# Kernel tuning notes

Hardware: AMD Instinct MI355X
Metric: run time of the kernel (lower is better)

Reference implementation:

```python
import jax, jax.numpy as jnp
import numpy as np

B, T, D, H, K = 4, 1024, 768, 12, 64
DMIX, DDEC = 32, 64

def setup_inputs() -> dict:
    key = jax.random.key(0)
    ks = jax.random.split(key, 24)
    def n(k, shape, s=1.0):
        return jax.random.normal(k, shape, dtype=jnp.float32) * s
    return {
        "x": n(ks[0], (B, T, D)),
        "time_maa_x": n(ks[1], (1, 1, D), 0.1) + 0.5,
        "time_maa_w": n(ks[2], (1, 1, D), 0.1) + 0.5,
        "time_maa_k": n(ks[3], (1, 1, D), 0.1) + 0.5,
        "time_maa_v": n(ks[4], (1, 1, D), 0.1) + 0.5,
        "time_maa_r": n(ks[5], (1, 1, D), 0.1) + 0.5,
        "time_maa_g": n(ks[6], (1, 1, D), 0.1) + 0.5,
        "maa_w1": n(ks[7], (D, 5 * DMIX), 0.01),
        "maa_w2": n(ks[8], (5, DMIX, D), 0.01),
        "time_decay": jnp.linspace(-6.0, -1.0, D).reshape(1, 1, D).astype(jnp.float32),
        "decay_w1": n(ks[9], (D, DDEC), 0.01),
        "decay_w2": n(ks[10], (DDEC, D), 0.01),
        "lucid_temp": jnp.ones((1, H, 1, 1), jnp.float32),
        "Wr": n(ks[11], (D, D), 0.02),
        "Wk": n(ks[12], (D, D), 0.02),
        "Wv": n(ks[13], (D, D), 0.02),
        "Wg": n(ks[14], (D, D), 0.02),
        "Wo": n(ks[15], (D, D), 0.02),
        "ln_w": jnp.ones((D,), jnp.float32),
        "ln_b": jnp.zeros((D,), jnp.float32),
    }

def reference(x, time_maa_x, time_maa_w, time_maa_k, time_maa_v, time_maa_r, time_maa_g,
              maa_w1, maa_w2, time_decay, decay_w1, decay_w2, lucid_temp,
              Wr, Wk, Wv, Wg, Wo, ln_w, ln_b):
    Bb, Tt, Dd = x.shape
    Hh = lucid_temp.shape[1]
    Kk = Dd // Hh
    # bidirectional token shift: average of left/right neighbors
    left = jnp.pad(x[:, :-1], ((0, 0), (1, 0), (0, 0)))
    right = jnp.pad(x[:, 1:], ((0, 0), (0, 1), (0, 0)))
    dxprev = 0.5 * (left + right) - x
    # data-dependent mixing coefficients (5-way low-rank)
    xxx = x + dxprev * time_maa_x
    m = jnp.tanh(xxx @ maa_w1).reshape(Bb, Tt, 5, DMIX)
    mm = jnp.einsum('btcd,cde->cbte', m, maa_w2)  # (5,B,T,D)
    mw, mk, mv, mr, mg = mm[0], mm[1], mm[2], mm[3], mm[4]
    xw = x + dxprev * (time_maa_w + mw)
    xk = x + dxprev * (time_maa_k + mk)
    xv = x + dxprev * (time_maa_v + mv)
    xr = x + dxprev * (time_maa_r + mr)
    xg = x + dxprev * (time_maa_g + mg)
    r = xr @ Wr
    k = xk @ Wk
    v = xv @ Wv
    g = jax.nn.silu(xg @ Wg)
    w = time_decay + jnp.tanh(xw @ decay_w1) @ decay_w2
    def heads(t):
        return t.reshape(Bb, Tt, Hh, Kk).transpose(0, 2, 1, 3)  # (B,H,T,K)
    r_h, k_h, v_h = heads(r), heads(k), heads(v)
    w_h = -jnp.exp(heads(w))
    # LION bidirectional decay attention
    cs = jnp.cumsum(w_h, axis=2)
    cs_b = cs - w_h
    cs_f_s = jnp.clip(cs - cs[:, :, Tt // 2:Tt // 2 + 1, :], -60.0, 60.0)
    cs_b_s = jnp.clip(cs_b - cs_b[:, :, Tt // 2:Tt // 2 + 1, :], -60.0, 60.0)
    A_fwd = jnp.tril(jnp.einsum('bhtk,bhsk->bhts', r_h * jnp.exp(cs_f_s), k_h * jnp.exp(-cs_f_s)))
    A_bwd = jnp.triu(jnp.einsum('bhtk,bhsk->bhts', r_h * jnp.exp(-cs_b_s), k_h * jnp.exp(cs_b_s)), 1)
    A = A_fwd + A_bwd
    # LUCID preconditioner: solve (I + exp(temp * K_norm K_norm^T)) Pv = v
    kn = k_h / jnp.maximum(jnp.linalg.norm(k_h, axis=-1, keepdims=True), 1e-12)
    gram = jnp.einsum('bhtk,bhsk->bhts', kn, kn)
    temp = jax.nn.softplus(lucid_temp)
    P = jnp.eye(Tt, dtype=jnp.float32) + jnp.exp(jnp.clip(temp * gram, -20.0, 20.0))
    Pv = jnp.linalg.solve(P, v_h)
    y = jnp.einsum('bhts,bhsk->bhtk', A, Pv)
    # GroupNorm over heads (groups = H, eps = 1e-5 * head_size_divisor^2)
    y = y.transpose(0, 2, 1, 3)  # (B,T,H,K)
    eps = 1e-5 * 64.0
    mu = y.mean(axis=-1, keepdims=True)
    var = y.var(axis=-1, keepdims=True)
    yn = (y - mu) / jnp.sqrt(var + eps)
    yn = yn.reshape(Bb, Tt, Dd) * ln_w + ln_b
    return (yn * g) @ Wo
```

## Files before the change

kernel.cpp:

```cpp
#include <hip/hip_runtime.h>
#include <math.h>

#define CB 4
#define CT 1024
#define CD 768
#define CH 12
#define CK 64
#define CBH (CB*CH)
#define NB 64

#define PTILE(i,j) ((size_t)(((i)*((i)+1))/2 + (j))*4096)
#define PBF ((size_t)136*4096)

typedef __attribute__((ext_vector_type(8))) short sh8;
typedef __attribute__((ext_vector_type(8))) unsigned short ush8;
typedef __attribute__((ext_vector_type(4))) unsigned short ush4;
typedef __attribute__((ext_vector_type(4))) float fl4;

__device__ __forceinline__ unsigned short f2bf(float f){
    unsigned u = __builtin_bit_cast(unsigned, f);
    unsigned r = (u + 0x7fff + ((u >> 16) & 1)) >> 16;
    return (unsigned short)r;
}
__device__ __forceinline__ float bf2f(unsigned short u){
    return __builtin_bit_cast(float, (unsigned)u << 16);
}
#define MFMA3(acc, ah, al, bh_, bl_) { \
    acc = __builtin_amdgcn_mfma_f32_16x16x32_bf16(al, bh_, acc, 0, 0, 0); \
    acc = __builtin_amdgcn_mfma_f32_16x16x32_bf16(ah, bl_, acc, 0, 0, 0); \
    acc = __builtin_amdgcn_mfma_f32_16x16x32_bf16(ah, bh_, acc, 0, 0, 0); }

#define LOAD_TILE(dst, src, stride) { \
    _Pragma("unroll") \
    for (int i_ = 0; i_ < 4; i_++){ \
        int rr_ = (tid>>4) + i_*16, cc_ = (tid&15)*4; \
        float4 v_ = *(const float4*)((src) + (size_t)rr_*(stride) + cc_); \
        dst[rr_][cc_+0]=v_.x; dst[rr_][cc_+1]=v_.y; dst[rr_][cc_+2]=v_.z; dst[rr_][cc_+3]=v_.w; \
    } }

__global__ void k_shift(const float* __restrict__ x, const float* __restrict__ tmx,
                        float* __restrict__ dxprev, float* __restrict__ xxx){
    int idx = blockIdx.x*256 + threadIdx.x;
    if (idx >= CB*CT*CD) return;
    int d = idx % CD;
    int bt = idx / CD;
    int t = bt % CT;
    float xc = x[idx];
    float xl = (t > 0)      ? x[idx - CD] : 0.f;
    float xr = (t < CT-1)   ? x[idx + CD] : 0.f;
    float dx = 0.5f*(xl + xr) - xc;
    dxprev[idx] = dx;
    xxx[idx] = xc + dx * tmx[d];
}

template<int MODE>
__global__ void k_gemm(const float* __restrict__ A, const float* __restrict__ Bm,
                       const float* __restrict__ bias, float* __restrict__ C,
                       int M, int N, int Kd){
    __shared__ float As[16][128];
    __shared__ float Bs[16][64];
    int tid = threadIdx.x;
    int m0 = blockIdx.y * 128, n0 = blockIdx.x * 64;
    int tn = (tid & 15) * 4;
    int tm = (tid >> 4) * 8;
    float acc[8][4] = {};
    for (int k0 = 0; k0 < Kd; k0 += 16){
        #pragma unroll
        for (int i = 0; i < 8; i++){
            int e = tid + i*256;
            int r = e >> 4, c = e & 15;
            As[c][r] = A[(size_t)(m0+r)*Kd + k0 + c];
        }
        #pragma unroll
        for (int i = 0; i < 4; i++){
            int e = tid + i*256;
            int r = e >> 6, c = e & 63;
            float bv = 0.f;
            if (n0 + c < N) bv = Bm[(size_t)(k0+r)*N + n0 + c];
            Bs[r][c] = bv;
        }
        __syncthreads();
        #pragma unroll
        for (int kk = 0; kk < 16; kk++){
            float a0[8], b0[4];
// ... 228 lines not shown
                       float* __restrict__ P, int bh0){
    int ti = blockIdx.y, tj = blockIdx.x;
    if (ti < tj) return;
    int t0 = ti*64, s0 = tj*64;
    __shared__ float tA[64][65];
    __shared__ float tB[64][65];
    int lbh = blockIdx.z; int gbh = bh0 + lbh; int h = gbh % CH;
    int tid = threadIdx.x;
    LOAD_TILE(tA, kn + ((size_t)gbh*CT + t0)*64, 64);
    LOAD_TILE(tB, kn + ((size_t)gbh*CT + s0)*64, 64);
    __syncthreads();
    float tv = lucid_temp[h];
    tv = (tv > 20.f) ? tv : log1pf(expf(tv));
    int ty = (tid >> 4)*4, tx = (tid & 15)*4;
    float acc[4][4] = {};
    #pragma unroll
    for (int kk = 0; kk < 64; kk++){
        float a0[4], b0[4];
        #pragma unroll
        for (int i = 0; i < 4; i++){ a0[i] = tA[ty+i][kk]; b0[i] = tB[tx+i][kk]; }
        #pragma unroll
        for (int i = 0; i < 4; i++)
            #pragma unroll
            for (int j = 0; j < 4; j++) acc[i][j] += a0[i]*b0[j];
    }
    float* Pt = P + (size_t)lbh*PBF + PTILE(ti,tj);
    #pragma unroll
    for (int i = 0; i < 4; i++){
        int tt = t0+ty+i;
        float4 v;
        float g0 = fminf(fmaxf(tv*acc[i][0], -20.f), 20.f);
        float g1 = fminf(fmaxf(tv*acc[i][1], -20.f), 20.f);
        float g2 = fminf(fmaxf(tv*acc[i][2], -20.f), 20.f);
        float g3 = fminf(fmaxf(tv*acc[i][3], -20.f), 20.f);
        v.x = expf(g0) + ((tt == s0+tx+0) ? 1.f : 0.f);
        v.y = expf(g1) + ((tt == s0+tx+1) ? 1.f : 0.f);
        v.z = expf(g2) + ((tt == s0+tx+2) ? 1.f : 0.f);
        v.w = expf(g3) + ((tt == s0+tx+3) ? 1.f : 0.f);
        *(float4*)(Pt + (size_t)(ty+i)*64 + tx) = v;
    }
}

__device__ __forceinline__ void potrf_inv(float (&s)[64][65], float (&inv)[64][65], int tid){
    for (int j = 0; j < 63; j++){
        __syncthreads();
        float invd = 1.f / fmaxf(s[j][j], 1e-20f);
        int n = 63 - j;
        for (int e = tid; e < n*n; e += 256){
            int ii = j+1 + e / n, cc = j+1 + e % n;
            s[ii][cc] -= s[ii][j]*s[cc][j]*invd;
        }
    }
    __syncthreads();
    for (int e = tid; e < 64*64; e += 256){
        int i2 = e >> 6, j2 = e & 63;
        if (i2 > j2) s[i2][j2] *= rsqrtf(fmaxf(s[j2][j2], 1e-20f));
    }
    __syncthreads();
    if (tid < 64) s[tid][tid] = sqrtf(fmaxf(s[tid][tid], 1e-20f));
    __syncthreads();
    if (tid < 64){
        int c = tid;
        for (int j = 0; j < c; j++) inv[j][c] = 0.f;
        for (int j = c; j < 64; j++){
            float sum = (j == c) ? 1.f : 0.f;
            for (int kk = c; kk < j; kk++) sum -= s[j][kk]*inv[kk][c];
            inv[j][c] = sum / s[j][j];
        }
    }
    __syncthreads();
}

__device__ __forceinline__ void potrf_writeout(float (&s)[64][65], float (&inv)[64][65], int tid,
                                               float* __restrict__ Pd, float* __restrict__ invp){
    for (int e = tid; e < 4096; e += 256){
        int r2 = e >> 6, c2 = e & 63;
        if (c2 <= r2) Pd[(size_t)r2*64 + c2] = s[r2][c2];
    }
    #pragma unroll
    for (int i_ = 0; i_ < 4; i_++){
        int rr_ = (tid>>4) + i_*16, cc_ = (tid&15)*4;
        float4 v_ = make_float4(inv[rr_][cc_], inv[rr_][cc_+1], inv[rr_][cc_+2], inv[rr_][cc_+3]);
        *(float4*)(invp + rr_*64 + cc_) = v_;
    }
}

__global__ void k_potrf0(float* __restrict__ P, float* __restrict__ invL){
    __shared__ float s[64][65], inv[64][65];
    int bh = blockIdx.x; int tid = threadIdx.x;
    float* Pt = P + (size_t)bh*PBF;
    LOAD_TILE(s, Pt, 64);
    __syncthreads();
    potrf_inv(s, inv, tid);
    potrf_writeout(s, inv, tid, Pt, invL + (size_t)bh*16*4096);
}

__global__ void k_trsm(float* __restrict__ P, const float* __restrict__ invL, int jb){
    __shared__ float a[64][65];
    __shared__ float iv[64][65];
    int bh = blockIdx.y;
    int rt = jb + 1 + blockIdx.x;
    int tid = threadIdx.x;
    float* Pt = P + (size_t)bh*PBF + PTILE(rt,jb);
    const float* invp = invL + ((size_t)bh*16 + jb)*4096;
    LOAD_TILE(a, Pt, 64);
    LOAD_TILE(iv, invp, 64);
    __syncthreads();
    int ty = (tid >> 4)*4, tx = (tid & 15)*4;
    float acc[4][4] = {};
    #pragma unroll
    for (int kk = 0; kk < 64; kk++){
        float a0[4], b0[4];
        #pragma unroll
        for (int i = 0; i < 4; i++){ a0[i] = a[ty+i][kk]; b0[i] = iv[tx+i][kk]; }
        #pragma unroll
        for (int i = 0; i < 4; i++)
            #pragma unroll
            for (int j = 0; j < 4; j++) acc[i][j] += a0[i]*b0[j];
    }
    #pragma unroll
    for (int i = 0; i < 4; i++)
        *(float4*)(Pt + (size_t)(ty+i)*64 + tx) =
            make_float4(acc[i][0], acc[i][1], acc[i][2], acc[i][3]);
}

__global__ void k_syrkf(float* __restrict__ P, float* __restrict__ invL,
                        float* __restrict__ X, float* __restrict__ Yb, int bh0, int jb){
    __shared__ float sA[64][65], sB[64][65], sC[64][65];
    int tj = blockIdx.x, ti = blockIdx.y, lbh = blockIdx.z;
    int tid = threadIdx.x;
    int ty = (tid >> 4)*4, tx = (tid & 15)*4;
    float* Pb = P + (size_t)lbh*PBF;
    if (tj == gridDim.x - 1){
        int ib = jb + 1 + ti;
        const float* invp = invL + ((size_t)lbh*16 + jb)*4096;
        const float* Xj = X + ((size_t)(bh0+lbh)*CT + jb*64)*64;
        LOAD_TILE(sA, invp, 64);
        LOAD_TILE(sB, Xj, 64);
        __syncthreads();
        float c4[4][4] = {};
        #pragma unroll
        for (int kk = 0; kk < 64; kk++){
            float a0[4], b0[4];
            #pragma unroll
            for (int i = 0; i < 4; i++){ a0[i] = sA[ty+i][kk]; b0[i] = sB[kk][tx+i]; }
            #pragma unroll
            for (int i = 0; i < 4; i++)
                #pragma unroll
                for (int j = 0; j < 4; j++) c4[i][j] += a0[i]*b0[j];
        }
        if (ti == 0){
            float* yd = Yb + ((size_t)(bh0+lbh)*CT + jb*64)*64;
            #pragma unroll
            for (int i = 0; i < 4; i++)
                *(float4*)(yd + (size_t)(ty+i)*64 + tx) =
                    make_float4(c4[i][0], c4[i][1], c4[i][2], c4[i][3]);
        }
        #pragma unroll
        for (int i = 0; i < 4; i++)
            #pragma unroll
            for (int j = 0; j < 4; j++) sC[ty+i][tx+j] = c4[i][j];
        __syncthreads();
        LOAD_TILE(sA, Pb + PTILE(ib,jb), 64);
        __syncthreads();
        float u4[4][4] = {};
        #pragma unroll
        for (int kk = 0; kk < 64; kk++){
            float a0[4], b0[4];
            #pragma unroll
            for (int i = 0; i < 4; i++){ a0[i] = sA[ty+i][kk]; b0[i] = sC[kk][tx+i]; }
            #pragma unroll
            for (int i = 0; i < 4; i++)
                #pragma unroll
                for (int j = 0; j < 4; j++) u4[i][j] += a0[i]*b0[j];
        }
        float* dst = X + ((size_t)(bh0+lbh)*CT + ib*64)*64;
        #pragma unroll
        for (int i = 0; i < 4; i++){
            float4* p4 = (float4*)(dst + (size_t)(ty+i)*64 + tx);
            float4 v = *p4;
            v.x -= u4[i][0]; v.y -= u4[i][1]; v.z -= u4[i][2]; v.w -= u4[i][3];
            *p4 = v;
        }
        return;
    }
    if (tj > ti) return;
    int ibr = jb + 1 + ti, ibc = jb + 1 + tj;
    LOAD_TILE(sA, Pb + PTILE(ibr,jb), 64);
    LOAD_TILE(sB, Pb + PTILE(ibc,jb), 64);
    __syncthreads();
    float acc[4][4] = {};
    #pragma unroll
    for (int kk = 0; kk < 64; kk++){
        float a0[4], b0[4];
        #pragma unroll
        for (int i = 0; i < 4; i++){ a0[i] = sA[ty+i][kk]; b0[i] = sB[tx+i][kk]; }
        #pragma unroll
        for (int i = 0; i < 4; i++)
            #pragma unroll
            for (int j = 0; j < 4; j++) acc[i][j] += a0[i]*b0[j];
    }
    if (!(ti == 0 && tj == 0)){
        float* Pt = Pb + PTILE(ibr,ibc);
        #pragma unroll
        for (int i = 0; i < 4; i++){
            float4* p4 = (float4*)(Pt + (size_t)(ty+i)*64 + tx);
            float4 v = *p4;
            v.x -= acc[i][0]; v.y -= acc[i][1]; v.z -= acc[i][2]; v.w -= acc[i][3];
            *p4 = v;
        }
    } else {
        float* Pt = Pb + PTILE(ibr,ibr);
        __syncthreads();
        #pragma unroll
        for (int i = 0; i < 4; i++){
            float4 v = *(const float4*)(Pt + (size_t)(ty+i)*64 + tx);
            sA[ty+i][tx+0] = v.x - acc[i][0];
            sA[ty+i][tx+1] = v.y - acc[i][1];
            sA[ty+i][tx+2] = v.z - acc[i][2];
            sA[ty+i][tx+3] = v.w - acc[i][3];
        }
        __syncthreads();
        potrf_inv(sA, sB, tid);
        potrf_writeout(sA, sB, tid, Pt, invL + ((size_t)lbh*16 + jb+1)*4096);
    }
}

template<int TRANS>
__global__ void k_solve(const float* __restrict__ P, const float* __restrict__ invL,
                        float* __restrict__ Xc, float* __restrict__ Yb, int bh0, int jb){
    __shared__ float A[64][65], B[64][65], C[64][65];
    int bh = blockIdx.y, tid = threadIdx.x;
    int ib = TRANS ? blockIdx.x : (jb + blockIdx.x);
    const float* invp = invL + ((size_t)bh*16 + jb)*4096;
    const float* src = (TRANS ? Yb : Xc) + ((size_t)(bh0+bh)*CT + jb*64)*64;
    LOAD_TILE(A, invp, 64);
    LOAD_TILE(B, src, 64);
    __syncthreads();
    int ty = (tid >> 4)*4, tx = (tid & 15)*4;
    float c4[4][4] = {};
    #pragma unroll
    for (int kk = 0; kk < 64; kk++){
        float a0[4], b0[4];
        #pragma unroll
        for (int i = 0; i < 4; i++){
            a0[i] = TRANS ? A[kk][ty+i] : A[ty+i][kk];
            b0[i] = B[kk][tx+i];
        }
        #pragma unroll
        for (int i = 0; i < 4; i++)
            #pragma unroll
            for (int j = 0; j < 4; j++) c4[i][j] += a0[i]*b0[j];
    }
    if (ib == jb){
        float* dst = (TRANS ? Xc : Yb) + ((size_t)(bh0+bh)*CT + jb*64)*64;
        #pragma unroll
        for (int i = 0; i < 4; i++)
            *(float4*)(dst + (size_t)(ty+i)*64 + tx) =
                make_float4(c4[i][0], c4[i][1], c4[i][2], c4[i][3]);
        return;
    }
    #pragma unroll
    for (int i = 0; i < 4; i++)
        #pragma unroll
        for (int j = 0; j < 4; j++) C[ty+i][tx+j] = c4[i][j];
    __syncthreads();
    const float* Lp = P + (size_t)bh*PBF + (TRANS ? PTILE(jb,ib) : PTILE(ib,jb));
    LOAD_TILE(A, Lp, 64);
    __syncthreads();
    float u4[4][4] = {};
    #pragma unroll
    for (int kk = 0; kk < 64; kk++){
        float a0[4], b0[4];
        #pragma unroll
        for (int i = 0; i < 4; i++){
            a0[i] = TRANS ? A[kk][ty+i] : A[ty+i][kk];
            b0[i] = C[kk][tx+i];
        }
        #pragma unroll
        for (int i = 0; i < 4; i++)
            #pragma unroll
            for (int j = 0; j < 4; j++) u4[i][j] += a0[i]*b0[j];
    }
    float* dst = (TRANS ? Yb : Xc) + ((size_t)(bh0+bh)*CT + ib*64)*64;
    #pragma unroll
    for (int i = 0; i < 4; i++){
        float4* p4 = (float4*)(dst + (size_t)(ty+i)*64 + tx);
        float4 v = *p4;
        v.x -= u4[i][0]; v.y -= u4[i][1]; v.z -= u4[i][2]; v.w -= u4[i][3];
        *p4 = v;
    }
}

__global__ void k_outer(const float* __restrict__ kf, const float* __restrict__ kb,
                        const float* __restrict__ X,
                        float* __restrict__ Sf, float* __restrict__ Sb){
    __shared__ float kfs[64][65], kbs[64][65], pvs[64][65];
    int c = blockIdx.x, bh = blockIdx.y, tid = threadIdx.x;
    size_t hb = (size_t)bh*CT*64 + (size_t)c*64*64;
    LOAD_TILE(kfs, kf + hb, 64);
    LOAD_TILE(kbs, kb + hb, 64);
    LOAD_TILE(pvs, X + hb, 64);
    __syncthreads();
    int ty = (tid >> 4)*4, tx = (tid & 15)*4;
    float af[4][4] = {}, ab[4][4] = {};
    #pragma unroll
    for (int kk = 0; kk < 64; kk++){
        float f0[4], g0[4], b0[4];
        #pragma unroll
        for (int i = 0; i < 4; i++){
            f0[i] = kfs[kk][ty+i];
            g0[i] = kbs[kk][ty+i];
            b0[i] = pvs[kk][tx+i];
        }
        #pragma unroll
        for (int i = 0; i < 4; i++)
            #pragma unroll
            for (int j = 0; j < 4; j++){
                af[i][j] += f0[i]*b0[j];
                ab[i][j] += g0[i]*b0[j];
            }
    }
    size_t sb = ((size_t)bh*16 + c)*4096;
    #pragma unroll
    for (int i = 0; i < 4; i++){
        *(float4*)(Sf + sb + (size_t)(ty+i)*64 + tx) = make_float4(af[i][0], af[i][1], af[i][2], af[i][3]);
        *(float4*)(Sb + sb + (size_t)(ty+i)*64 + tx) = make_float4(ab[i][0], ab[i][1], ab[i][2], ab[i][3]);
    }
}

__global__ void k_cumsum(float* __restrict__ Sf, float* __restrict__ Sb){
    int bh = blockIdx.x, tid = threadIdx.x;
    size_t base = (size_t)bh*16*4096;
    #pragma unroll
    for (int i = 0; i < 16; i++){
        int e = tid + i*256;
        float run = 0.f;
        for (int c = 0; c < 16; c++){
            float* p = Sf + base + (size_t)c*4096 + e;
            float t = *p; *p = run; run += t;
        }
        run = 0.f;
        for (int c = 15; c >= 0; c--){
            float* p = Sb + base + (size_t)c*4096 + e;
            float t = *p; *p = run; run += t;
        }
    }
}

__global__ void k_apv2(const float* __restrict__ rf, const float* __restrict__ kf,
                       const float* __restrict__ rb, const float* __restrict__ kb,
                       const float* __restrict__ X,
                       const float* __restrict__ Sf, const float* __restrict__ Sb,
                       float* __restrict__ y){
    __shared__ float rs[64][65], ks[64][65], at[64][65];
    int c = blockIdx.x, bh = blockIdx.y, tid = threadIdx.x;
    size_t hb = (size_t)bh*CT*64 + (size_t)c*64*64;
    size_t sb = ((size_t)bh*16 + c)*4096;
    int ty = (tid >> 4)*4, tx = (tid & 15)*4;
    LOAD_TILE(rs, rf + hb, 64);
    LOAD_TILE(ks, kf + hb, 64);
    __syncthreads();
    float a4[4][4] = {};
    #pragma unroll
    for (int kk = 0; kk < 64; kk++){
        float a0[4], b0[4];
        #pragma unroll
        for (int i = 0; i < 4; i++){ a0[i] = rs[ty+i][kk]; b0[i] = ks[tx+i][kk]; }
        #pragma unroll
        for (int i = 0; i < 4; i++)
            #pragma unroll
            for (int j = 0; j < 4; j++) a4[i][j] += a0[i]*b0[j];
    }
    __syncthreads();
// ... 44 lines not shown
            #pragma unroll
            for (int j = 0; j < 4; j++) yacc[i][j] += a0[i]*b0[j];
    }
    __syncthreads();
    LOAD_TILE(rs, Sb + sb, 64);
    LOAD_TILE(ks, rb + hb, 64);
    __syncthreads();
    #pragma unroll 8
    for (int kk = 0; kk < 64; kk++){
        float a0[4], b0[4];
        #pragma unroll
        for (int i = 0; i < 4; i++){ a0[i] = ks[ty+i][kk]; b0[i] = rs[kk][tx+i]; }
        #pragma unroll
        for (int i = 0; i < 4; i++)
            #pragma unroll
            for (int j = 0; j < 4; j++) yacc[i][j] += a0[i]*b0[j];
    }
    #pragma unroll
    for (int i = 0; i < 4; i++)
        *(float4*)(y + hb + (size_t)(ty+i)*64 + tx) =
            make_float4(yacc[i][0], yacc[i][1], yacc[i][2], yacc[i][3]);
}

__global__ void k_gn(const float* __restrict__ y, const float* __restrict__ g,
                     const float* __restrict__ lnw, const float* __restrict__ lnb,
                     float* __restrict__ z){
    int gw = (blockIdx.x*256 + threadIdx.x) >> 6;
    int lane = threadIdx.x & 63;
    if (gw >= CB*CT*CH) return;
    int h = gw % CH; int bt = gw / CH;
    int b = bt / CT, t = bt % CT;
    int bh = b*CH + h;
    float yv = y[((size_t)bh*CT + t)*64 + lane];
    float s1 = yv, s2 = yv*yv;
    #pragma unroll
    for (int off = 32; off; off >>= 1){ s1 += __shfl_xor(s1, off); s2 += __shfl_xor(s2, off); }
    float mu = s1 * (1.f/64.f);
    float var = s2 * (1.f/64.f) - mu*mu;
    float inv = rsqrtf(var + 6.4e-4f);
    int d = h*64 + lane;
    float yn = (yv - mu)*inv*lnw[d] + lnb[d];
    z[(size_t)bt*CD + d] = yn * g[(size_t)bt*CD + d];
}

extern "C" void kernel_launch(void* const* d_in, const int* in_sizes, int n_in,
                              void* d_out, int out_size, void* d_ws, size_t ws_size,
                              hipStream_t stream){
    const float* x          = (const float*)d_in[0];
    const float* tmx        = (const float*)d_in[1];
    const float* tmw        = (const float*)d_in[2];
    const float* tmk        = (const float*)d_in[3];
    const float* tmv        = (const float*)d_in[4];
    const float* tmr        = (const float*)d_in[5];
    const float* tmg        = (const float*)d_in[6];
    const float* maa_w1     = (const float*)d_in[7];
    const float* maa_w2     = (const float*)d_in[8];
    const float* time_decay = (const float*)d_in[9];
    const float* decay_w1   = (const float*)d_in[10];
    const float* decay_w2   = (const float*)d_in[11];
    const float* lucid_temp = (const float*)d_in[12];
    const float* Wr         = (const float*)d_in[13];
    const float* Wk         = (const float*)d_in[14];
    const float* Wv         = (const float*)d_in[15];
    const float* Wg         = (const float*)d_in[16];
    const float* Wo         = (const float*)d_in[17];
    const float* lnw        = (const float*)d_in[18];
    const float* lnb        = (const float*)d_in[19];
    float* out = (float*)d_out;
    float* ws  = (float*)d_ws;

    const size_t S = (size_t)CB*CT*CD;
    float* b0 = ws;
    float* b1 = ws + 1*S;
    float* b2 = ws + 2*S;
    float* b3 = ws + 3*S;
    float* b4 = ws + 4*S;
    float* b5 = ws + 5*S;
    float* b6 = ws + 6*S;
    float* b7 = ws + 7*S;
    float* b8 = ws + 8*S;
    float* b9 = ws + 9*S;
    float* mbuf = ws + 10*S;
    const size_t MB_F = 4096*160;
    size_t base_f = 10*S + MB_F;

    const size_t per_bh = PBF + 16*4096;
    size_t avail = ws_size / sizeof(float);
    int G = 1;
    if (avail > base_f + per_bh){
        size_t g = (avail - base_f) / per_bh;
        G = (g >= CBH) ? CBH : (int)g;
        if (G < 1) G = 1;
    }
    float* P    = ws + base_f;
    float* invL = P + (size_t)G*PBF;

    unsigned short* BtHi = (unsigned short*)P;
    unsigned short* BtLo = BtHi + (size_t)CD*CD;

    float* dxprev = b0; float* xxx = b1;
    float* xw = b1; float* xk = b2; float* xv = b3; float* xr = b4; float* xg = b5;
    float* rbuf = b6; float* kbuf = b7; float* vbuf = b8; float* gbuf = b9; float* wbuf = b0;
    float* kn = b4; float* X = b5;
    float* rf = b1; float* kf = b2; float* rb = b3; float* kb = b8;
    float* Yb = b0;
    float* Sf = b4; float* Sb = b0;
    float* ybuf = b6; float* zbuf = b7;

    dim3 mg(CD/64, (CB*CT)/64);
    dim3 tg(CD/64, CD/64);

    k_shift<<<dim3((CB*CT*CD + 255)/256), 256, 0, stream>>>(x, tmx, dxprev, xxx);
    k_gemm<1><<<dim3(3, 32), 256, 0, stream>>>(xxx, maa_w1, nullptr, mbuf, 4096, 160, 768);
    k_mix5<<<dim3(3, 4096), 256, 0, stream>>>(x, dxprev, mbuf, tmw, tmk, tmv, tmr, tmg,
                                              maa_w2, xw, xk, xv, xr, xg);
    k_splitT<<<tg, 256, 0, stream>>>(Wr, BtHi, BtLo, CD, CD);
    k_mgemm<0><<<mg, 256, 0, stream>>>(xr, BtHi, BtLo, nullptr, rbuf, 4096, CD, CD);
    k_splitT<<<tg, 256, 0, stream>>>(Wk, BtHi, BtLo, CD, CD);
    k_mgemm<0><<<mg, 256, 0, stream>>>(xk, BtHi, BtLo, nullptr, kbuf, 4096, CD, CD);
    k_splitT<<<tg, 256, 0, stream>>>(Wv, BtHi, BtLo, CD, CD);
    k_mgemm<0><<<mg, 256, 0, stream>>>(xv, BtHi, BtLo, nullptr, vbuf, 4096, CD, CD);
    k_splitT<<<tg, 256, 0, stream>>>(Wg, BtHi, BtLo, CD, CD);
    k_mgemm<2><<<mg, 256, 0, stream>>>(xg, BtHi, BtLo, nullptr, gbuf, 4096, CD, CD);
    k_splitT<<<dim3(1, 12), 256, 0, stream>>>(decay_w1, BtHi, BtLo, CD, 64);
    k_mgemm<1><<<dim3(1, 64), 256, 0, stream>>>(xw, BtHi, BtLo, nullptr, mbuf, 4096, 64, CD);
    k_splitT<<<dim3(12, 1), 256, 0, stream>>>(decay_w2, BtHi, BtLo, 64, CD);
    k_mgemm<3><<<dim3(12, 64), 256, 0, stream>>>(mbuf, BtHi, BtLo, time_decay, wbuf, 4096, CD, 64);

    k_knvx<<<dim3((CB*CH*CT*64)/256), 256, 0, stream>>>(kbuf, vbuf, kn, X);
    k_scan2<<<dim3(CBH), 256, 0, stream>>>(rbuf, kbuf, wbuf, rf, kf, rb, kb);

    for (int bh0 = 0; bh0 < CBH; bh0 += G){
        int Gc = (CBH - bh0 < G) ? (CBH - bh0) : G;
        k_gram<<<dim3(16, 16, Gc), 256, 0, stream>>>(kn, lucid_temp, P, bh0);
        k_potrf0<<<dim3(Gc), 256, 0, stream>>>(P, invL);
        for (int jb = 0; jb < 15; jb++){
            int nt = 15 - jb;
            k_trsm<<<dim3(nt, Gc), 256, 0, stream>>>(P, invL, jb);
            k_syrkf<<<dim3(nt+1, nt, Gc), 256, 0, stream>>>(P, invL, X, Yb, bh0, jb);
        }
        k_solve<0><<<dim3(1, Gc), 256, 0, stream>>>(P, invL, X, Yb, bh0, 15);
        for (int jb = 15; jb >= 0; jb--)
            k_solve<1><<<dim3(jb+1, Gc), 256, 0, stream>>>(P, invL, X, Yb, bh0, jb);
    }

    k_outer<<<dim3(16, CBH), 256, 0, stream>>>(kf, kb, X, Sf, Sb);
    k_cumsum<<<dim3(CBH), 256, 0, stream>>>(Sf, Sb);
    k_apv2<<<dim3(16, CBH), 256, 0, stream>>>(rf, kf, rb, kb, X, Sf, Sb, ybuf);
    k_gn<<<dim3((CB*CT*CH*64)/256), 256, 0, stream>>>(ybuf, gbuf, lnw, lnb, zbuf);
    k_splitT<<<tg, 256, 0, stream>>>(Wo, BtHi, BtLo, CD, CD);
    k_mgemm<0><<<mg, 256, 0, stream>>>(zbuf, BtHi, BtLo, nullptr, out, 4096, CD, CD);
}
```

Measured before the change: 3.330 ms.

## Fuse blocked Cholesky and triangular solves into one cooperative persistent kernel

Replaces the sequence of small per-step launches (potrf, trsm, syrk and forward/backward solve per block column) with one cooperative kernel. It loops over phases and uses grid-wide syncs between them, removing many tiny kernel launches and their launch gaps. In exchange, each phase spins on grid barriers, occupancy is limited by three 64x65 shared tiles per block, and the cooperative launch falls back to the old path if it fails.

Result: no change. 3.329 ms (-0.0%).

```diff
diff --git a/kernel.cpp b/kernel.cpp
--- a/kernel.cpp
+++ b/kernel.cpp
@@ -1,5 +1,8 @@
 #include <hip/hip_runtime.h>
+#include <hip/hip_cooperative_groups.h>
 #include <math.h>
+
+namespace cg = cooperative_groups;
 
 #define CB 4
 #define CT 1024
@@ -394,6 +397,240 @@
         int rr_ = (tid>>4) + i_*16, cc_ = (tid&15)*4;
         float4 v_ = make_float4(inv[rr_][cc_], inv[rr_][cc_+1], inv[rr_][cc_+2], inv[rr_][cc_+3]);
         *(float4*)(invp + rr_*64 + cc_) = v_;
+    }
+}
+
+__global__ __launch_bounds__(256) void k_chol(float* __restrict__ P, float* __restrict__ invL,
+                                              float* __restrict__ X, float* __restrict__ Yb,
+                                              int bh0, int Gc){
+    cg::grid_group gg = cg::this_grid();
+    __shared__ float sA[64][65], sB[64][65], sC[64][65];
+    int tid = threadIdx.x;
+    int ty = (tid >> 4)*4, tx = (tid & 15)*4;
+    int NBK = gridDim.x, blk = blockIdx.x;
+
+    for (int t = blk; t < Gc; t += NBK){
+        float* Pt = P + (size_t)t*PBF;
+        LOAD_TILE(sA, Pt, 64);
+        __syncthreads();
+        potrf_inv(sA, sB, tid);
+        potrf_writeout(sA, sB, tid, Pt, invL + (size_t)t*16*4096);
+        __syncthreads();
+    }
+    gg.sync();
+
+    for (int jb = 0; jb < 15; jb++){
+        int nt = 15 - jb;
+        for (int t = blk; t < Gc*nt; t += NBK){
+            int bh = t / nt, ti = t % nt;
+            int rt = jb + 1 + ti;
+            float* Pt = P + (size_t)bh*PBF + PTILE(rt,jb);
+            const float* invp = invL + ((size_t)bh*16 + jb)*4096;
+            LOAD_TILE(sA, Pt, 64);
+            LOAD_TILE(sB, invp, 64);
+            __syncthreads();
+            float acc[4][4] = {};
+            #pragma unroll
+            for (int kk = 0; kk < 64; kk++){
+                float a0[4], b0[4];
+                #pragma unroll
+                for (int i = 0; i < 4; i++){ a0[i] = sA[ty+i][kk]; b0[i] = sB[tx+i][kk]; }
+                #pragma unroll
+                for (int i = 0; i < 4; i++)
+                    #pragma unroll
+                    for (int j = 0; j < 4; j++) acc[i][j] += a0[i]*b0[j];
+            }
+            __syncthreads();
+            #pragma unroll
+            for (int i = 0; i < 4; i++)
+                *(float4*)(Pt + (size_t)(ty+i)*64 + tx) =
+                    make_float4(acc[i][0], acc[i][1], acc[i][2], acc[i][3]);
+        }
+        gg.sync();
+        int Wd = nt + 1;
+        for (int t = blk; t < Gc*nt*Wd; t += NBK){
+            int bh = t / (nt*Wd); int r = t % (nt*Wd);
+            int ti = r / Wd, tj = r % Wd;
+            float* Pb = P + (size_t)bh*PBF;
+            if (tj == nt){
+                int ib = jb + 1 + ti;
+                const float* invp = invL + ((size_t)bh*16 + jb)*4096;
+                const float* Xj = X + ((size_t)(bh0+bh)*CT + jb*64)*64;
+                LOAD_TILE(sA, invp, 64);
+                LOAD_TILE(sB, Xj, 64);
+                __syncthreads();
+                float c4[4][4] = {};
+                #pragma unroll
+                for (int kk = 0; kk < 64; kk++){
+                    float a0[4], b0[4];
+                    #pragma unroll
+                    for (int i = 0; i < 4; i++){ a0[i] = sA[ty+i][kk]; b0[i] = sB[kk][tx+i]; }
+                    #pragma unroll
+                    for (int i = 0; i < 4; i++)
+                        #pragma unroll
+                        for (int j = 0; j < 4; j++) c4[i][j] += a0[i]*b0[j];
+                }
+                if (ti == 0){
+                    float* yd = Yb + ((size_t)(bh0+bh)*CT + jb*64)*64;
+                    #pragma unroll
+                    for (int i = 0; i < 4; i++)
+                        *(float4*)(yd + (size_t)(ty+i)*64 + tx) =
+                            make_float4(c4[i][0], c4[i][1], c4[i][2], c4[i][3]);
+                }
+                #pragma unroll
+                for (int i = 0; i < 4; i++)
+                    #pragma unroll
+                    for (int j = 0; j < 4; j++) sC[ty+i][tx+j] = c4[i][j];
+                __syncthreads();
+                LOAD_TILE(sA, Pb + PTILE(ib,jb), 64);
+                __syncthreads();
+                float u4[4][4] = {};
+                #pragma unroll
+                for (int kk = 0; kk < 64; kk++){
+                    float a0[4], b0[4];
+                    #pragma unroll
+                    for (int i = 0; i < 4; i++){ a0[i] = sA[ty+i][kk]; b0[i] = sC[kk][tx+i]; }
+                    #pragma unroll
+                    for (int i = 0; i < 4; i++)
+                        #pragma unroll
+                        for (int j = 0; j < 4; j++) u4[i][j] += a0[i]*b0[j];
+                }
+                float* dst = X + ((size_t)(bh0+bh)*CT + ib*64)*64;
+                #pragma unroll
+                for (int i = 0; i < 4; i++){
+                    float4* p4 = (float4*)(dst + (size_t)(ty+i)*64 + tx);
+                    float4 v = *p4;
+                    v.x -= u4[i][0]; v.y -= u4[i][1]; v.z -= u4[i][2]; v.w -= u4[i][3];
+                    *p4 = v;
+                }
+                __syncthreads();
+            } else if (tj <= ti){
+                int ibr = jb + 1 + ti, ibc = jb + 1 + tj;
+                LOAD_TILE(sA, Pb + PTILE(ibr,jb), 64);
+                LOAD_TILE(sB, Pb + PTILE(ibc,jb), 64);
+                __syncthreads();
+                float acc[4][4] = {};
+                #pragma unroll
+                for (int kk = 0; kk < 64; kk++){
+                    float a0[4], b0[4];
+                    #pragma unroll
+                    for (int i = 0; i < 4; i++){ a0[i] = sA[ty+i][kk]; b0[i] = sB[tx+i][kk]; }
+                    #pragma unroll
+                    for (int i = 0; i < 4; i++)
+                        #pragma unroll
+                        for (int j = 0; j < 4; j++) acc[i][j] += a0[i]*b0[j];
+                }
+                __syncthreads();
+                if (!(ti == 0 && tj == 0)){
+                    float* Pt = Pb + PTILE(ibr,ibc);
+                    #pragma unroll
+                    for (int i = 0; i < 4; i++){
+                        float4* p4 = (float4*)(Pt + (size_t)(ty+i)*64 + tx);
+                        float4 v = *p4;
+                        v.x -= acc[i][0]; v.y -= acc[i][1]; v.z -= acc[i][2]; v.w -= acc[i][3];
+                        *p4 = v;
+                    }
+                } else {
+                    float* Pt = Pb + PTILE(ibr,ibr);
+                    #pragma unroll
+                    for (int i = 0; i < 4; i++){
+                        float4 v = *(const float4*)(Pt + (size_t)(ty+i)*64 + tx);
+                        sA[ty+i][tx+0] = v.x - acc[i][0];
+                        sA[ty+i][tx+1] = v.y - acc[i][1];
+                        sA[ty+i][tx+2] = v.z - acc[i][2];
+                        sA[ty+i][tx+3] = v.w - acc[i][3];
+                    }
+                    __syncthreads();
+                    potrf_inv(sA, sB, tid);
+                    potrf_writeout(sA, sB, tid, Pt, invL + ((size_t)bh*16 + jb+1)*4096);
+                    __syncthreads();
+                }
+            }
+        }
+        gg.sync();
+    }
+    for (int t = blk; t < Gc; t += NBK){
+        const float* invp = invL + ((size_t)t*16 + 15)*4096;
+        const float* Xj = X + ((size_t)(bh0+t)*CT + 15*64)*64;
+        LOAD_TILE(sA, invp, 64);
+        LOAD_TILE(sB, Xj, 64);
+        __syncthreads();
+        float c4[4][4] = {};
+        #pragma unroll
+        for (int kk = 0; kk < 64; kk++){
+            float a0[4], b0[4];
+            #pragma unroll
+            for (int i = 0; i < 4; i++){ a0[i] = sA[ty+i][kk]; b0[i] = sB[kk][tx+i]; }
+            #pragma unroll
+            for (int i = 0; i < 4; i++)
+                #pragma unroll
+                for (int j = 0; j < 4; j++) c4[i][j] += a0[i]*b0[j];
+        }
+        __syncthreads();
+        float* yd = Yb + ((size_t)(bh0+t)*CT + 15*64)*64;
+        #pragma unroll
+        for (int i = 0; i < 4; i++)
+            *(float4*)(yd + (size_t)(ty+i)*64 + tx) =
+                make_float4(c4[i][0], c4[i][1], c4[i][2], c4[i][3]);
+    }
+    gg.sync();
+    for (int jb = 15; jb >= 0; jb--){
+        for (int t = blk; t < Gc*(jb+1); t += NBK){
+            int bh = t / (jb+1), ib = t % (jb+1);
+            const float* invp = invL + ((size_t)bh*16 + jb)*4096;
+            const float* src = Yb + ((size_t)(bh0+bh)*CT + jb*64)*64;
+            LOAD_TILE(sA, invp, 64);
+            LOAD_TILE(sB, src, 64);
+            __syncthreads();
+            float c4[4][4] = {};
+            #pragma unroll
+            for (int kk = 0; kk < 64; kk++){
+                float a0[4], b0[4];
+                #pragma unroll
+                for (int i = 0; i < 4; i++){ a0[i] = sA[kk][ty+i]; b0[i] = sB[kk][tx+i]; }
+                #pragma unroll
+                for (int i = 0; i < 4; i++)
+                    #pragma unroll
+                    for (int j = 0; j < 4; j++) c4[i][j] += a0[i]*b0[j];
+            }
+            if (ib == jb){
+                float* dst = X + ((size_t)(bh0+bh)*CT + jb*64)*64;
+                #pragma unroll
+                for (int i = 0; i < 4; i++)
+                    *(float4*)(dst + (size_t)(ty+i)*64 + tx) =
+                        make_float4(c4[i][0], c4[i][1], c4[i][2], c4[i][3]);
+                __syncthreads();
+            } else {
+                #pragma unroll
+                for (int i = 0; i < 4; i++)
+                    #pragma unroll
+                    for (int j = 0; j < 4; j++) sC[ty+i][tx+j] = c4[i][j];
+                __syncthreads();
+                LOAD_TILE(sA, P + (size_t)bh*PBF + PTILE(jb,ib), 64);
+                __syncthreads();
+                float u4[4][4] = {};
+                #pragma unroll
+                for (int kk = 0; kk < 64; kk++){
+                    float a0[4], b0[4];
+                    #pragma unroll
+                    for (int i = 0; i < 4; i++){ a0[i] = sA[kk][ty+i]; b0[i] = sC[kk][tx+i]; }
+                    #pragma unroll
+                    for (int i = 0; i < 4; i++)
+                        #pragma unroll
+                        for (int j = 0; j < 4; j++) u4[i][j] += a0[i]*b0[j];
+                }
+                float* dst = Yb + ((size_t)(bh0+bh)*CT + ib*64)*64;
+                #pragma unroll
+                for (int i = 0; i < 4; i++){
+                    float4* p4 = (float4*)(dst + (size_t)(ty+i)*64 + tx);
+                    float4 v = *p4;
+                    v.x -= u4[i][0]; v.y -= u4[i][1]; v.z -= u4[i][2]; v.w -= u4[i][3];
+                    *p4 = v;
+                }
+                __syncthreads();
+            }
+        }
+        gg.sync();
     }
 }
 
@@ -860,18 +1097,39 @@
     k_knvx<<<dim3((CB*CH*CT*64)/256), 256, 0, stream>>>(kbuf, vbuf, kn, X);
     k_scan2<<<dim3(CBH), 256, 0, stream>>>(rbuf, kbuf, wbuf, rf, kf, rb, kb);
 
+    int devId = 0;
+    hipGetDevice(&devId);
+    hipDeviceProp_t prop;
+    hipGetDeviceProperties(&prop, devId);
+    int maxB = 0;
+    hipError_t occErr = hipOccupancyMaxActiveBlocksPerMultiprocessor(&maxB, k_chol, 256, 0);
+    int nblk = (occErr == hipSuccess && maxB > 0) ? maxB * prop.multiProcessorCount : 0;
+    if (nblk > 2048) nblk = 2048;
+
     for (int bh0 = 0; bh0 < CBH; bh0 += G){
         int Gc = (CBH - bh0 < G) ? (CBH - bh0) : G;
         k_gram<<<dim3(16, 16, Gc), 256, 0, stream>>>(kn, lucid_temp, P, bh0);
-        k_potrf0<<<dim3(Gc), 256, 0, stream>>>(P, invL);
-        for (int jb = 0; jb < 15; jb++){
-            int nt = 15 - jb;
-            k_trsm<<<dim3(nt, Gc), 256, 0, stream>>>(P, invL, jb);
-            k_syrkf<<<dim3(nt+1, nt, Gc), 256, 0, stream>>>(P, invL, X, Yb, bh0, jb);
-        }
-        k_solve<0><<<dim3(1, Gc), 256, 0, stream>>>(P, invL, X, Yb, bh0, 15);
-        for (int jb = 15; jb >= 0; jb--)
-            k_solve<1><<<dim3(jb+1, Gc), 256, 0, stream>>>(P, invL, X, Yb, bh0, jb);
+        bool done = false;
+        if (nblk >= 64){
+            int bh0a = bh0, gca = Gc;
+            void* args[] = {(void*)&P, (void*)&invL, (void*)&X, (void*)&Yb,
+                            (void*)&bh0a, (void*)&gca};
+            hipError_t e = hipLaunchCooperativeKernel((void*)k_chol, dim3(nblk), dim3(256),
+                                                      args, 0, stream);
+            done = (e == hipSuccess);
+            if (!done) (void)hipGetLastError();
+        }
+        if (!done){
+            k_potrf0<<<dim3(Gc), 256, 0, stream>>>(P, invL);
+            for (int jb = 0; jb < 15; jb++){
+                int nt = 15 - jb;
+                k_trsm<<<dim3(nt, Gc), 256, 0, stream>>>(P, invL, jb);
+                k_syrkf<<<dim3(nt+1, nt, Gc), 256, 0, stream>>>(P, invL, X, Yb, bh0, jb);
+            }
+            k_solve<0><<<dim3(1, Gc), 256, 0, stream>>>(P, invL, X, Yb, bh0, 15);
+            for (int jb = 15; jb >= 0; jb--)
+                k_solve<1><<<dim3(jb+1, Gc), 256, 0, stream>>>(P, invL, X, Yb, bh0, jb);
+        }
     }
 
     k_outer<<<dim3(16, CBH), 256, 0, stream>>>(kf, kb, X, Sf, Sb);
```

## Fuse blocked Cholesky factorization and solves into one persistent kernel

Applied to the files above, without the earlier changes.

Replaces the per-step launches of potrf, trsm, syrk and the forward/backward triangular solves with a single persistent kernel. It uses 16 workgroups per (batch, head) that synchronise through global atomic counter barriers. This removes dozens of small kernel launches and their launch gaps per batch chunk. In exchange it relies on all workgroups being co-resident: a hand-rolled spin barrier, with limited parallelism of 16 blocks per head and idle blocks in later steps.

Measured after the change: 7.511 ms. +125.5%, slower.

```diff
diff --git a/kernel.cpp b/kernel.cpp
--- a/kernel.cpp
+++ b/kernel.cpp
@@ -397,58 +397,173 @@
     }
 }
 
-__global__ void k_potrf0(float* __restrict__ P, float* __restrict__ invL){
-    __shared__ float s[64][65], inv[64][65];
-    int bh = blockIdx.x; int tid = threadIdx.x;
-    float* Pt = P + (size_t)bh*PBF;
-    LOAD_TILE(s, Pt, 64);
-    __syncthreads();
-    potrf_inv(s, inv, tid);
-    potrf_writeout(s, inv, tid, Pt, invL + (size_t)bh*16*4096);
-}
-
-__global__ void k_trsm(float* __restrict__ P, const float* __restrict__ invL, int jb){
-    __shared__ float a[64][65];
-    __shared__ float iv[64][65];
-    int bh = blockIdx.y;
-    int rt = jb + 1 + blockIdx.x;
-    int tid = threadIdx.x;
-    float* Pt = P + (size_t)bh*PBF + PTILE(rt,jb);
-    const float* invp = invL + ((size_t)bh*16 + jb)*4096;
-    LOAD_TILE(a, Pt, 64);
-    LOAD_TILE(iv, invp, 64);
-    __syncthreads();
-    int ty = (tid >> 4)*4, tx = (tid & 15)*4;
-    float acc[4][4] = {};
-    #pragma unroll
-    for (int kk = 0; kk < 64; kk++){
-        float a0[4], b0[4];
-        #pragma unroll
-        for (int i = 0; i < 4; i++){ a0[i] = a[ty+i][kk]; b0[i] = iv[tx+i][kk]; }
-        #pragma unroll
-        for (int i = 0; i < 4; i++)
-            #pragma unroll
-            for (int j = 0; j < 4; j++) acc[i][j] += a0[i]*b0[j];
-    }
-    #pragma unroll
-    for (int i = 0; i < 4; i++)
-        *(float4*)(Pt + (size_t)(ty+i)*64 + tx) =
-            make_float4(acc[i][0], acc[i][1], acc[i][2], acc[i][3]);
-}
-
-__global__ void k_syrkf(float* __restrict__ P, float* __restrict__ invL,
-                        float* __restrict__ X, float* __restrict__ Yb, int bh0, int jb){
+__global__ void k_zflags(int* __restrict__ flags){
+    flags[blockIdx.x*256 + threadIdx.x] = 0;
+}
+
+__global__ __launch_bounds__(256, 3) void k_fact(float* __restrict__ P, float* __restrict__ invL,
+        float* __restrict__ X, float* __restrict__ Yb, int* __restrict__ flags,
+        int bh0, int Gc){
+    int gid = blockIdx.x >> 4;
+    int r   = blockIdx.x & 15;
+    if (gid >= Gc) return;
     __shared__ float sA[64][65], sB[64][65], sC[64][65];
-    int tj = blockIdx.x, ti = blockIdx.y, lbh = blockIdx.z;
     int tid = threadIdx.x;
     int ty = (tid >> 4)*4, tx = (tid & 15)*4;
-    float* Pb = P + (size_t)lbh*PBF;
-    if (tj == gridDim.x - 1){
-        int ib = jb + 1 + ti;
-        const float* invp = invL + ((size_t)lbh*16 + jb)*4096;
-        const float* Xj = X + ((size_t)(bh0+lbh)*CT + jb*64)*64;
-        LOAD_TILE(sA, invp, 64);
-        LOAD_TILE(sB, Xj, 64);
+    float* Pb   = P + (size_t)gid*PBF;
+    float* invb = invL + (size_t)gid*16*4096;
+    float* Xb   = X  + (size_t)(bh0+gid)*CT*64;
+    float* Yg   = Yb + (size_t)(bh0+gid)*CT*64;
+    int* cnt = flags + gid*64;
+    int ph = 0;
+#define GBAR() { __syncthreads(); \
+    if (tid == 0){ __threadfence(); atomicAdd(&cnt[ph], 1); \
+        while (__hip_atomic_load(&cnt[ph], __ATOMIC_ACQUIRE, __HIP_MEMORY_SCOPE_AGENT) < 16) \
+            __builtin_amdgcn_s_sleep(2); \
+        __threadfence(); } \
+    __syncthreads(); ph++; }
+
+    if (r == 0){
+        LOAD_TILE(sA, Pb, 64);
+        __syncthreads();
+        potrf_inv(sA, sB, tid);
+        potrf_writeout(sA, sB, tid, Pb, invb);
+    }
+    GBAR();
+
+    for (int jb = 0; jb < 15; jb++){
+        int nt = 15 - jb;
+        if (r < nt){
+            int rt = jb + 1 + r;
+            float* Pt = Pb + PTILE(rt,jb);
+            const float* invp = invb + jb*4096;
+            LOAD_TILE(sA, Pt, 64);
+            LOAD_TILE(sB, invp, 64);
+            __syncthreads();
+            float acc[4][4] = {};
+            #pragma unroll
+            for (int kk = 0; kk < 64; kk++){
+                float a0[4], b0[4];
+                #pragma unroll
+                for (int i = 0; i < 4; i++){ a0[i] = sA[ty+i][kk]; b0[i] = sB[tx+i][kk]; }
+                #pragma unroll
+                for (int i = 0; i < 4; i++)
+                    #pragma unroll
+                    for (int j = 0; j < 4; j++) acc[i][j] += a0[i]*b0[j];
+            }
+            __syncthreads();
+            #pragma unroll
+            for (int i = 0; i < 4; i++)
+                *(float4*)(Pt + (size_t)(ty+i)*64 + tx) =
+                    make_float4(acc[i][0], acc[i][1], acc[i][2], acc[i][3]);
+        }
+        GBAR();
+        int npair = nt*(nt+1)/2;
+        int ntask = npair + nt;
+        for (int t = r; t < ntask; t += 16){
+            if (t >= npair){
+                int ib = jb + 1 + (t - npair);
+                LOAD_TILE(sA, invb + jb*4096, 64);
+                LOAD_TILE(sB, Xb + (size_t)(jb*64)*64, 64);
+                __syncthreads();
+                float c4[4][4] = {};
+                #pragma unroll
+                for (int kk = 0; kk < 64; kk++){
+                    float a0[4], b0[4];
+                    #pragma unroll
+                    for (int i = 0; i < 4; i++){ a0[i] = sA[ty+i][kk]; b0[i] = sB[kk][tx+i]; }
+                    #pragma unroll
+                    for (int i = 0; i < 4; i++)
+                        #pragma unroll
+                        for (int j = 0; j < 4; j++) c4[i][j] += a0[i]*b0[j];
+                }
+                if (t == npair){
+                    float* yd = Yg + (size_t)(jb*64)*64;
+                    #pragma unroll
+                    for (int i = 0; i < 4; i++)
+                        *(float4*)(yd + (size_t)(ty+i)*64 + tx) =
+                            make_float4(c4[i][0], c4[i][1], c4[i][2], c4[i][3]);
+                }
+                #pragma unroll
+                for (int i = 0; i < 4; i++)
+                    #pragma unroll
+                    for (int j = 0; j < 4; j++) sC[ty+i][tx+j] = c4[i][j];
+                __syncthreads();
+                LOAD_TILE(sA, Pb + PTILE(ib,jb), 64);
+                __syncthreads();
+                float u4[4][4] = {};
+                #pragma unroll
+                for (int kk = 0; kk < 64; kk++){
+                    float a0[4], b0[4];
+                    #pragma unroll
+                    for (int i = 0; i < 4; i++){ a0[i] = sA[ty+i][kk]; b0[i] = sC[kk][tx+i]; }
+                    #pragma unroll
+                    for (int i = 0; i < 4; i++)
+                        #pragma unroll
+                        for (int j = 0; j < 4; j++) u4[i][j] += a0[i]*b0[j];
+                }
+                float* dst = Xb + (size_t)(ib*64)*64;
+                #pragma unroll
+                for (int i = 0; i < 4; i++){
+                    float4* p4 = (float4*)(dst + (size_t)(ty+i)*64 + tx);
+                    float4 v = *p4;
+                    v.x -= u4[i][0]; v.y -= u4[i][1]; v.z -= u4[i][2]; v.w -= u4[i][3];
+                    *p4 = v;
+                }
+                __syncthreads();
+            } else {
+                int ti = 0;
+                while (((ti+1)*(ti+2))/2 <= t) ti++;
+                int tj = t - (ti*(ti+1))/2;
+                int ibr = jb + 1 + ti, ibc = jb + 1 + tj;
+                LOAD_TILE(sA, Pb + PTILE(ibr,jb), 64);
+                LOAD_TILE(sB, Pb + PTILE(ibc,jb), 64);
+                __syncthreads();
+                float acc[4][4] = {};
+                #pragma unroll
+                for (int kk = 0; kk < 64; kk++){
+                    float a0[4], b0[4];
+                    #pragma unroll
+                    for (int i = 0; i < 4; i++){ a0[i] = sA[ty+i][kk]; b0[i] = sB[tx+i][kk]; }
+                    #pragma unroll
+                    for (int i = 0; i < 4; i++)
+                        #pragma unroll
+                        for (int j = 0; j < 4; j++) acc[i][j] += a0[i]*b0[j];
+                }
+                __syncthreads();
+                if (t != 0){
+                    float* Pt = Pb + PTILE(ibr,ibc);
+                    #pragma unroll
+                    for (int i = 0; i < 4; i++){
+                        float4* p4 = (float4*)(Pt + (size_t)(ty+i)*64 + tx);
+                        float4 v = *p4;
+                        v.x -= acc[i][0]; v.y -= acc[i][1]; v.z -= acc[i][2]; v.w -= acc[i][3];
+                        *p4 = v;
+                    }
+                    __syncthreads();
+                } else {
+                    float* Pt = Pb + PTILE(ibr,ibr);
+                    #pragma unroll
+                    for (int i = 0; i < 4; i++){
+                        float4 v = *(const float4*)(Pt + (size_t)(ty+i)*64 + tx);
+                        sA[ty+i][tx+0] = v.x - acc[i][0];
+                        sA[ty+i][tx+1] = v.y - acc[i][1];
+                        sA[ty+i][tx+2] = v.z - acc[i][2];
+                        sA[ty+i][tx+3] = v.w - acc[i][3];
+                    }
+                    __syncthreads();
+                    potrf_inv(sA, sB, tid);
+                    potrf_writeout(sA, sB, tid, Pt, invb + (jb+1)*4096);
+                    __syncthreads();
+                }
+            }
+        }
+        GBAR();
+    }
+
+    if (r == 0){
+        LOAD_TILE(sA, invb + 15*4096, 64);
+        LOAD_TILE(sB, Xb + (size_t)(15*64)*64, 64);
         __syncthreads();
         float c4[4][4] = {};
         #pragma unroll
@@ -461,147 +576,71 @@
                 #pragma unroll
                 for (int j = 0; j < 4; j++) c4[i][j] += a0[i]*b0[j];
         }
-        if (ti == 0){
-            float* yd = Yb + ((size_t)(bh0+lbh)*CT + jb*64)*64;
-            #pragma unroll
-            for (int i = 0; i < 4; i++)
-                *(float4*)(yd + (size_t)(ty+i)*64 + tx) =
-                    make_float4(c4[i][0], c4[i][1], c4[i][2], c4[i][3]);
-        }
+        __syncthreads();
+        float* yd = Yg + (size_t)(15*64)*64;
         #pragma unroll
         for (int i = 0; i < 4; i++)
-            #pragma unroll
-            for (int j = 0; j < 4; j++) sC[ty+i][tx+j] = c4[i][j];
-        __syncthreads();
-        LOAD_TILE(sA, Pb + PTILE(ib,jb), 64);
-        __syncthreads();
-        float u4[4][4] = {};
-        #pragma unroll
-        for (int kk = 0; kk < 64; kk++){
-            float a0[4], b0[4];
-            #pragma unroll
-            for (int i = 0; i < 4; i++){ a0[i] = sA[ty+i][kk]; b0[i] = sC[kk][tx+i]; }
-            #pragma unroll
-            for (int i = 0; i < 4; i++)
-                #pragma unroll
-                for (int j = 0; j < 4; j++) u4[i][j] += a0[i]*b0[j];
-        }
-        float* dst = X + ((size_t)(bh0+lbh)*CT + ib*64)*64;
-        #pragma unroll
-        for (int i = 0; i < 4; i++){
-            float4* p4 = (float4*)(dst + (size_t)(ty+i)*64 + tx);
-            float4 v = *p4;
-            v.x -= u4[i][0]; v.y -= u4[i][1]; v.z -= u4[i][2]; v.w -= u4[i][3];
-            *p4 = v;
-        }
-        return;
-    }
-    if (tj > ti) return;
-    int ibr = jb + 1 + ti, ibc = jb + 1 + tj;
-    LOAD_TILE(sA, Pb + PTILE(ibr,jb), 64);
-    LOAD_TILE(sB, Pb + PTILE(ibc,jb), 64);
-    __syncthreads();
-    float acc[4][4] = {};
-    #pragma unroll
-    for (int kk = 0; kk < 64; kk++){
-        float a0[4], b0[4];
-        #pragma unroll
-        for (int i = 0; i < 4; i++){ a0[i] = sA[ty+i][kk]; b0[i] = sB[tx+i][kk]; }
-        #pragma unroll
-        for (int i = 0; i < 4; i++)
-            #pragma unroll
-            for (int j = 0; j < 4; j++) acc[i][j] += a0[i]*b0[j];
-    }
-    if (!(ti == 0 && tj == 0)){
-        float* Pt = Pb + PTILE(ibr,ibc);
-        #pragma unroll
-        for (int i = 0; i < 4; i++){
-            float4* p4 = (float4*)(Pt + (size_t)(ty+i)*64 + tx);
-            float4 v = *p4;
-            v.x -= acc[i][0]; v.y -= acc[i][1]; v.z -= acc[i][2]; v.w -= acc[i][3];
-            *p4 = v;
-        }
-    } else {
-        float* Pt = Pb + PTILE(ibr,ibr);
-        __syncthreads();
-        #pragma unroll
-        for (int i = 0; i < 4; i++){
-            float4 v = *(const float4*)(Pt + (size_t)(ty+i)*64 + tx);
-            sA[ty+i][tx+0] = v.x - acc[i][0];
-            sA[ty+i][tx+1] = v.y - acc[i][1];
-            sA[ty+i][tx+2] = v.z - acc[i][2];
-            sA[ty+i][tx+3] = v.w - acc[i][3];
-        }
-        __syncthreads();
-        potrf_inv(sA, sB, tid);
-        potrf_writeout(sA, sB, tid, Pt, invL + ((size_t)lbh*16 + jb+1)*4096);
-    }
-}
-
-template<int TRANS>
-__global__ void k_solve(const float* __restrict__ P, const float* __restrict__ invL,
-                        float* __restrict__ Xc, float* __restrict__ Yb, int bh0, int jb){
-    __shared__ float A[64][65], B[64][65], C[64][65];
-    int bh = blockIdx.y, tid = threadIdx.x;
-    int ib = TRANS ? blockIdx.x : (jb + blockIdx.x);
-    const float* invp = invL + ((size_t)bh*16 + jb)*4096;
-    const float* src = (TRANS ? Yb : Xc) + ((size_t)(bh0+bh)*CT + jb*64)*64;
-    LOAD_TILE(A, invp, 64);
-    LOAD_TILE(B, src, 64);
-    __syncthreads();
-    int ty = (tid >> 4)*4, tx = (tid & 15)*4;
-    float c4[4][4] = {};
-    #pragma unroll
-    for (int kk = 0; kk < 64; kk++){
-        float a0[4], b0[4];
-        #pragma unroll
-        for (int i = 0; i < 4; i++){
-            a0[i] = TRANS ? A[kk][ty+i] : A[ty+i][kk];
-            b0[i] = B[kk][tx+i];
-        }
-        #pragma unroll
-        for (int i = 0; i < 4; i++)
-            #pragma unroll
-            for (int j = 0; j < 4; j++) c4[i][j] += a0[i]*b0[j];
-    }
-    if (ib == jb){
-        float* dst = (TRANS ? Xc : Yb) + ((size_t)(bh0+bh)*CT + jb*64)*64;
-        #pragma unroll
-        for (int i = 0; i < 4; i++)
-            *(float4*)(dst + (size_t)(ty+i)*64 + tx) =
+            *(float4*)(yd + (size_t)(ty+i)*64 + tx) =
                 make_float4(c4[i][0], c4[i][1], c4[i][2], c4[i][3]);
-        return;
-    }
-    #pragma unroll
-    for (int i = 0; i < 4; i++)
-        #pragma unroll
-        for (int j = 0; j < 4; j++) C[ty+i][tx+j] = c4[i][j];
-    __syncthreads();
-    const float* Lp = P + (size_t)bh*PBF + (TRANS ? PTILE(jb,ib) : PTILE(ib,jb));
-    LOAD_TILE(A, Lp, 64);
-    __syncthreads();
-    float u4[4][4] = {};
-    #pragma unroll
-    for (int kk = 0; kk < 64; kk++){
-        float a0[4], b0[4];
-        #pragma unroll
-        for (int i = 0; i < 4; i++){
-            a0[i] = TRANS ? A[kk][ty+i] : A[ty+i][kk];
-            b0[i] = C[kk][tx+i];
-        }
-        #pragma unroll
-        for (int i = 0; i < 4; i++)
-            #pragma unroll
-            for (int j = 0; j < 4; j++) u4[i][j] += a0[i]*b0[j];
-    }
-    float* dst = (TRANS ? Yb : Xc) + ((size_t)(bh0+bh)*CT + ib*64)*64;
-    #pragma unroll
-    for (int i = 0; i < 4; i++){
-        float4* p4 = (float4*)(dst + (size_t)(ty+i)*64 + tx);
-        float4 v = *p4;
-        v.x -= u4[i][0]; v.y -= u4[i][1]; v.z -= u4[i][2]; v.w -= u4[i][3];
-        *p4 = v;
-    }
+    }
+    GBAR();
+
+    for (int jb = 15; jb >= 0; jb--){
+        for (int ib = r; ib <= jb; ib += 16){
+            LOAD_TILE(sA, invb + jb*4096, 64);
+            LOAD_TILE(sB, Yg + (size_t)(jb*64)*64, 64);
+            __syncthreads();
+            float c4[4][4] = {};
+            #pragma unroll
+            for (int kk = 0; kk < 64; kk++){
+                float a0[4], b0[4];
+                #pragma unroll
+                for (int i = 0; i < 4; i++){ a0[i] = sA[kk][ty+i]; b0[i] = sB[kk][tx+i]; }
+                #pragma unroll
+                for (int i = 0; i < 4; i++)
+                    #pragma unroll
+                    for (int j = 0; j < 4; j++) c4[i][j] += a0[i]*b0[j];
+            }
+            if (ib == jb){
+                float* dst = Xb + (size_t)(jb*64)*64;
+                #pragma unroll
+                for (int i = 0; i < 4; i++)
+                    *(float4*)(dst + (size_t)(ty+i)*64 + tx) =
+                        make_float4(c4[i][0], c4[i][1], c4[i][2], c4[i][3]);
+                __syncthreads();
+            } else {
+                #pragma unroll
+                for (int i = 0; i < 4; i++)
+                    #pragma unroll
+                    for (int j = 0; j < 4; j++) sC[ty+i][tx+j] = c4[i][j];
+                __syncthreads();
+                LOAD_TILE(sA, Pb + PTILE(jb,ib), 64);
+                __syncthreads();
+                float u4[4][4] = {};
+                #pragma unroll
+                for (int kk = 0; kk < 64; kk++){
+                    float a0[4], b0[4];
+                    #pragma unroll
+                    for (int i = 0; i < 4; i++){ a0[i] = sA[kk][ty+i]; b0[i] = sC[kk][tx+i]; }
+                    #pragma unroll
+                    for (int i = 0; i < 4; i++)
+                        #pragma unroll
+                        for (int j = 0; j < 4; j++) u4[i][j] += a0[i]*b0[j];
+                }
+                float* dst = Yg + (size_t)(ib*64)*64;
+                #pragma unroll
+                for (int i = 0; i < 4; i++){
+                    float4* p4 = (float4*)(dst + (size_t)(ty+i)*64 + tx);
+                    float4 v = *p4;
+                    v.x -= u4[i][0]; v.y -= u4[i][1]; v.z -= u4[i][2]; v.w -= u4[i][3];
+                    *p4 = v;
+                }
+                __syncthreads();
+            }
+        }
+        GBAR();
+    }
+#undef GBAR
 }
 
 __global__ void k_outer(const float* __restrict__ kf, const float* __restrict__ kb,
@@ -812,17 +851,21 @@
     float* b9 = ws + 9*S;
     float* mbuf = ws + 10*S;
     const size_t MB_F = 4096*160;
+    const size_t FLAGS_F = 4096;
     size_t base_f = 10*S + MB_F;
+
+    int* flags = (int*)(ws + base_f);
+    size_t pool_f = base_f + FLAGS_F;
 
     const size_t per_bh = PBF + 16*4096;
     size_t avail = ws_size / sizeof(float);
     int G = 1;
-    if (avail > base_f + per_bh){
-        size_t g = (avail - base_f) / per_bh;
+    if (avail > pool_f + per_bh){
+        size_t g = (avail - pool_f) / per_bh;
         G = (g >= CBH) ? CBH : (int)g;
         if (G < 1) G = 1;
     }
-    float* P    = ws + base_f;
+    float* P    = ws + pool_f;
     float* invL = P + (size_t)G*PBF;
 
     unsigned short* BtHi = (unsigned short*)P;
@@ -863,15 +906,8 @@
     for (int bh0 = 0; bh0 < CBH; bh0 += G){
         int Gc = (CBH - bh0 < G) ? (CBH - bh0) : G;
         k_gram<<<dim3(16, 16, Gc), 256, 0, stream>>>(kn, lucid_temp, P, bh0);
-        k_potrf0<<<dim3(Gc), 256, 0, stream>>>(P, invL);
-        for (int jb = 0; jb < 15; jb++){
-            int nt = 15 - jb;
-            k_trsm<<<dim3(nt, Gc), 256, 0, stream>>>(P, invL, jb);
-            k_syrkf<<<dim3(nt+1, nt, Gc), 256, 0, stream>>>(P, invL, X, Yb, bh0, jb);
-        }
-        k_solve<0><<<dim3(1, Gc), 256, 0, stream>>>(P, invL, X, Yb, bh0, 15);
-        for (int jb = 15; jb >= 0; jb--)
-            k_solve<1><<<dim3(jb+1, Gc), 256, 0, stream>>>(P, invL, X, Yb, bh0, jb);
+        k_zflags<<<dim3(12), 256, 0, stream>>>(flags);
+        k_fact<<<dim3(Gc*16), 256, 0, stream>>>(P, invL, X, Yb, flags, bh0, Gc);
     }
 
     k_outer<<<dim3(16, CBH), 256, 0, stream>>>(kf, kb, X, Sf, Sb);
```
